# Kernel tuning notes

Measured on AMD Instinct MI355X. Metric: run time of the kernel, lower is better.

## Reference

```python
import jax, jax.numpy as jnp
import numpy as np
import math

N_ANGLES = 8
HIGH_FREQ_RATIO = 0.3


def setup_inputs() -> dict:
    key = jax.random.key(0)
    k1, k2 = jax.random.split(key)
    x = jax.random.normal(k1, (4, 256, 256, 256), dtype=jnp.float32)
    # learnable per-angle weights, init near enhance_init=1.0 with small perturbation
    angle_weights = 1.0 + 0.1 * jax.random.normal(k2, (N_ANGLES,), dtype=jnp.float32)
    return {"x": x, "angle_weights": angle_weights}


def _angle_gain(H, W, angle_weights):
    # Build [H, W] real gain: angle-sector weight in the high-frequency band, 1 elsewhere.
    cy, cx = H // 2, W // 2
    y = jnp.arange(H, dtype=jnp.float32)[:, None] - cy
    x = jnp.arange(W, dtype=jnp.float32)[None, :] - cx
    r = jnp.sqrt(y * y + x * x)
    theta = jnp.arctan2(y, x) + math.pi  # [0, 2*pi]
    angle_step = 2.0 * math.pi / N_ANGLES
    angle_idx = jnp.mod(jnp.floor(theta / angle_step).astype(jnp.int32), N_ANGLES)
    r_max = min(cy, cx)
    high_freq_mask = r > HIGH_FREQ_RATIO * r_max
    weights = angle_weights[angle_idx]  # [H, W]
    return jnp.where(high_freq_mask, weights, jnp.ones_like(weights))


def reference(x, angle_weights):
    # x: [B, C, H, W]
    H, W = x.shape[-2], x.shape[-1]
    gain = _angle_gain(H, W, angle_weights)  # [H, W], real
    xf = jnp.fft.fftshift(jnp.fft.fft2(x, norm="ortho"), axes=(-2, -1))
    # mag*gain * exp(i*phase) == gain * (mag*exp(i*phase)) == gain * spectrum (gain real)
    xf_enh = xf * gain
    x_enh = jnp.fft.ifft2(jnp.fft.ifftshift(xf_enh, axes=(-2, -1)), norm="ortho").real
    return x + x_enh
```

## Files before the change

kernel.cpp:

```cpp
#include <hip/hip_runtime.h>
#include <math.h>

#define PI_F 3.14159265358979323846f
#define WSYNC() asm volatile("s_waitcnt lgkmcnt(0)" ::: "memory")

__device__ __forceinline__ float2 cmul(float2 a, float2 b) {
    return make_float2(a.x * b.x - a.y * b.y, a.x * b.y + a.y * b.x);
}
__device__ __forceinline__ float2 cmulc(float2 a, float2 b) {
    return make_float2(a.x * b.x + a.y * b.y, a.y * b.x - a.x * b.y);
}
__device__ __forceinline__ int digitrev4(int p) {
    return ((p & 3) << 6) | (((p >> 2) & 3) << 4) | (((p >> 4) & 3) << 2) | ((p >> 6) & 3);
}
__device__ __forceinline__ int bitrev8(int p) {
    return (int)(__brev((unsigned int)p) >> 24);
}
__device__ __forceinline__ int SW(int i) { return i ^ ((i >> 4) & 15); }

__device__ __forceinline__ void tw3(int eu, float2& w1, float2& w2, float2& w3) {
    float sn, cs;
    __sincosf(-(2.0f * PI_F / 256.0f) * (float)eu, &sn, &cs);
    w1 = make_float2(cs, sn);
    w2 = cmul(w1, w1);
    w3 = cmul(w2, w1);
}

__device__ __forceinline__ void bfly4_fwd(float2 a0, float2 a1, float2 a2, float2 a3,
                                          float2& o0, float2& o1, float2& o2, float2& o3) {
    float2 t0 = make_float2(a0.x + a2.x, a0.y + a2.y);
    float2 t1 = make_float2(a0.x - a2.x, a0.y - a2.y);
    float2 t2 = make_float2(a1.x + a3.x, a1.y + a3.y);
    float2 u  = make_float2(a1.x - a3.x, a1.y - a3.y);
    float2 t3 = make_float2(u.y, -u.x);
    o0 = make_float2(t0.x + t2.x, t0.y + t2.y);
    o1 = make_float2(t1.x + t3.x, t1.y + t3.y);
    o2 = make_float2(t0.x - t2.x, t0.y - t2.y);
    o3 = make_float2(t1.x - t3.x, t1.y - t3.y);
}
__device__ __forceinline__ void bfly4_inv(float2 a0, float2 a1, float2 a2, float2 a3,
                                          float2& o0, float2& o1, float2& o2, float2& o3) {
    float2 t0 = make_float2(a0.x + a2.x, a0.y + a2.y);
    float2 t1 = make_float2(a0.x - a2.x, a0.y - a2.y);
    float2 t2 = make_float2(a1.x + a3.x, a1.y + a3.y);
    float2 u  = make_float2(a1.x - a3.x, a1.y - a3.y);
    float2 t3 = make_float2(-u.y, u.x);
    o0 = make_float2(t0.x + t2.x, t0.y + t2.y);
    o1 = make_float2(t1.x + t3.x, t1.y + t3.y);
    o2 = make_float2(t0.x - t2.x, t0.y - t2.y);
    o3 = make_float2(t1.x - t3.x, t1.y - t3.y);
}

template<int S>
__device__ __forceinline__ void stage_fwd_j(float2* line, int j, float2 w1, float2 w2, float2 w3) {
    const int h = 1 << (2 * S);
    int k  = j & (h - 1);
    int i0 = ((j >> (2 * S)) << (2 * S + 2)) + k;
    int p0 = SW(i0), p1 = SW(i0 + h), p2 = SW(i0 + 2 * h), p3 = SW(i0 + 3 * h);
    float2 a0 = line[p0], a1 = line[p1], a2 = line[p2], a3 = line[p3];
    float2 o0, o1, o2, o3;
    bfly4_fwd(a0, a1, a2, a3, o0, o1, o2, o3);
    line[p0] = o0;
    line[p1] = cmul(o1, w1);
    line[p2] = cmul(o2, w2);
    line[p3] = cmul(o3, w3);
}
template<int S>
__device__ __forceinline__ void stage_inv_j(float2* line, int j, float2 w1, float2 w2, float2 w3) {
    const int h = 1 << (2 * S);
    int k  = j & (h - 1);
    int i0 = ((j >> (2 * S)) << (2 * S + 2)) + k;
    int p0 = SW(i0), p1 = SW(i0 + h), p2 = SW(i0 + 2 * h), p3 = SW(i0 + 3 * h);
    float2 b0 = line[p0];
    float2 b1 = cmulc(line[p1], w1);
    float2 b2 = cmulc(line[p2], w2);
    float2 b3 = cmulc(line[p3], w3);
    float2 o0, o1, o2, o3;
    bfly4_inv(b0, b1, b2, b3, o0, o1, o2, o3);
    line[p0] = o0; line[p1] = o1; line[p2] = o2; line[p3] = o3;
}

template<int MB>
__device__ __forceinline__ void xs_fwd(float2* a, float2* b, int lane,
                                       float step, float cC, float sC) {
    float dm = (lane & MB) ? 1.0f : 0.0f;
    float s  = 1.0f - 2.0f * dm;
    float ang = step * dm * (float)(lane & (MB - 1));
    float sn, cs; __sincosf(ang, &sn, &cs);
    float2 tw = make_float2(cs, sn);
    float2 Cm = make_float2(1.0f + dm * (cC - 1.0f), dm * sC);
#pragma unroll
    for (int d = 0; d < 4; ++d) {
        float tax = __shfl_xor(a[d].x, MB), tay = __shfl_xor(a[d].y, MB);
        float tbx = __shfl_xor(b[d].x, MB), tby = __shfl_xor(b[d].y, MB);
        float2 ra = make_float2(tax + s * a[d].x, tay + s * a[d].y);
        float2 rb = make_float2(tbx + s * b[d].x, tby + s * b[d].y);
        a[d] = cmul(ra, tw);
        b[d] = cmul(rb, tw);
        tw = cmul(tw, Cm);
    }
}
template<int MB>
__device__ __forceinline__ void xs_inv(float2* a, float2* b, int lane,
                                       float step, float cC, float sC) {
    float dm = (lane & MB) ? 1.0f : 0.0f;
    float s  = 1.0f - 2.0f * dm;
    float ang = step * dm * (float)(lane & (MB - 1));
    float sn, cs; __sincosf(ang, &sn, &cs);
    float2 tw = make_float2(cs, sn);
    float2 Cm = make_float2(1.0f + dm * (cC - 1.0f), dm * sC);
#pragma unroll
    for (int d = 0; d < 4; ++d) {
        float2 pa = cmul(a[d], tw);
        float2 pb = cmul(b[d], tw);
        float tax = __shfl_xor(pa.x, MB), tay = __shfl_xor(pa.y, MB);
        float tbx = __shfl_xor(pb.x, MB), tby = __shfl_xor(pb.y, MB);
        a[d] = make_float2(tax + s * pa.x, tay + s * pa.y);
        b[d] = make_float2(tbx + s * pb.x, tby + s * pb.y);
        tw = cmul(tw, Cm);
    }
}
__device__ __forceinline__ void local_fwd(float2* v) {
    float2 u0 = make_float2(v[0].x + v[2].x, v[0].y + v[2].y);
    float2 u2 = make_float2(v[0].x - v[2].x, v[0].y - v[2].y);
    float2 u1 = make_float2(v[1].x + v[3].x, v[1].y + v[3].y);
    float2 w  = make_float2(v[1].x - v[3].x, v[1].y - v[3].y);
    float2 u3 = make_float2(w.y, -w.x);
    v[0] = make_float2(u0.x + u1.x, u0.y + u1.y);
    v[1] = make_float2(u0.x - u1.x, u0.y - u1.y);
    v[2] = make_float2(u2.x + u3.x, u2.y + u3.y);
    v[3] = make_float2(u2.x - u3.x, u2.y - u3.y);
}
__device__ __forceinline__ void local_inv(float2* v) {
    float2 u0 = make_float2(v[0].x + v[1].x, v[0].y + v[1].y);
    float2 u1 = make_float2(v[0].x - v[1].x, v[0].y - v[1].y);
    float2 u2 = make_float2(v[2].x + v[3].x, v[2].y + v[3].y);
    float2 u3 = make_float2(v[2].x - v[3].x, v[2].y - v[3].y);
    float2 w  = make_float2(-u3.y, u3.x);
    v[0] = make_float2(u0.x + u2.x, u0.y + u2.y);
    v[2] = make_float2(u0.x - u2.x, u0.y - u2.y);
    v[1] = make_float2(u1.x + w.x, u1.y + w.y);
    v[3] = make_float2(u1.x - w.x, u1.y - w.y);
}

__device__ __forceinline__ float gain1(float fy, float fx, const float* sw) {
    float r2 = fy * fy + fx * fx;
    float theta = atan2f(fy, fx) + PI_F;
    int idx = ((int)floorf(theta * (4.0f / PI_F))) & 7;
    float wv = sw[idx];
    return (r2 > 1474.56f) ? wv : 1.0f;
}

__global__ __launch_bounds__(256) void k_gain_lut(const float* __restrict__ wts, float* __restrict__ lut2) {
    __shared__ float sw[8];
    int h = threadIdx.x, w = blockIdx.x;
    if (h < 8) sw[h] = wts[h];
    __syncthreads();
    int kw = bitrev8(w), kh = digitrev4(h);
    float fx  = (kw < 128) ? (float)kw : (float)(kw - 256);
    float fx2 = (kw == 128) ? -128.0f : -fx;
    float fy  = (kh < 128) ? (float)kh : (float)(kh - 256);
    float fy2 = (kh == 128) ? -128.0f : -fy;
    float g1 = gain1(fy, fx, sw);
    float g2 = gain1(fy2, fx2, sw);
    lut2[w * 256 + h] = (1.0f + 0.5f * (g1 + g2)) * (1.0f / 65536.0f);
}

__global__ __launch_bounds__(256) void k_row_fwd(const float* __restrict__ x, float* __restrict__ out) {
    int t = threadIdx.x, wv = t >> 6, lane = t & 63;
    int gr = blockIdx.x * 8 + wv * 2;
    int q = gr >> 8, h = gr & 255;
    int plane = ((q >> 7) << 8) + ((q & 127) << 1);
    size_t rA = ((size_t)plane << 16) + ((size_t)h << 8);
    size_t rB = rA + 65536;
    int w4 = lane * 4;
    float4 re0 = *(const float4*)(x + rA + w4);
    float4 im0 = *(const float4*)(x + rB + w4);
    float4 re1 = *(const float4*)(x + rA + 256 + w4);
    float4 im1 = *(const float4*)(x + rB + 256 + w4);
    float2 a[4], b[4];
    a[0] = make_float2(re0.x, im0.x); a[1] = make_float2(re0.y, im0.y);
    a[2] = make_float2(re0.z, im0.z); a[3] = make_float2(re0.w, im0.w);
    b[0] = make_float2(re1.x, im1.x); b[1] = make_float2(re1.y, im1.y);
    b[2] = make_float2(re1.z, im1.z); b[3] = make_float2(re1.w, im1.w);
    xs_fwd<32>(a, b, lane, -0.09817477f, 0.99969882f, -0.02454123f);
    xs_fwd<16>(a, b, lane, -0.19634954f, 0.99879546f, -0.04906767f);
    xs_fwd< 8>(a, b, lane, -0.39269908f, 0.99518473f, -0.09801714f);
    xs_fwd< 4>(a, b, lane, -0.78539816f, 0.98078528f, -0.19509032f);
    xs_fwd< 2>(a, b, lane, -1.57079633f, 0.92387953f, -0.38268343f);
    xs_fwd< 1>(a, b, lane, -3.14159265f, 0.70710678f, -0.70710678f);
    local_fwd(a); local_fwd(b);
    *(float4*)(out + rA + w4)       = make_float4(a[0].x, a[1].x, a[2].x, a[3].x);
    *(float4*)(out + rB + w4)       = make_float4(a[0].y, a[1].y, a[2].y, a[3].y);
    *(float4*)(out + rA + 256 + w4) = make_float4(b[0].x, b[1].x, b[2].x, b[3].x);
    *(float4*)(out + rB + 256 + w4) = make_float4(b[0].y, b[1].y, b[2].y, b[3].y);
}

template<bool USE_LUT>
__global__ __launch_bounds__(256) void k_col(float* __restrict__ data,
                                             const float* __restrict__ lut2,
                                             const float* __restrict__ wts) {
    __shared__ float2 tile[16][256];
    int t = threadIdx.x;
    int q = blockIdx.x >> 4, wt = blockIdx.x & 15, w0 = wt * 16;
    int plane = ((q >> 7) << 8) + ((q & 127) << 1);
    size_t baseA = ((size_t)plane << 16) + (size_t)w0;
    size_t baseB = baseA + 65536;
    int c0 = (t & 3) * 4, h0 = (t >> 2) * 4;
    int wv = t >> 6, lane = t & 63;
    int i0 = lane * 4;

    float4 gAr[2], gBr[2];
    if (!USE_LUT) {
        if (t < 8) ((float*)tile)[t] = wts[t];
        __syncthreads();
        const float* swp = (const float*)tile;
#pragma unroll
        for (int cp = 0; cp < 2; ++cp) {
#pragma unroll
            for (int cc = 0; cc < 2; ++cc) {
                int col = wv * 4 + cp * 2 + cc;
                int kw = bitrev8(w0 + col);
                float fx  = (kw < 128) ? (float)kw : (float)(kw - 256);
                float fx2 = (kw == 128) ? -128.0f : -fx;
                float4 g;
#pragma unroll
                for (int d = 0; d < 4; ++d) {
                    int kh = digitrev4(i0 + d);
                    float fy  = (kh < 128) ? (float)kh : (float)(kh - 256);
                    float fy2 = (kh == 128) ? -128.0f : -fy;
                    float g1v = gain1(fy, fx, swp);
                    float g2v = gain1(fy2, fx2, swp);
                    (&g.x)[d] = (1.0f + 0.5f * (g1v + g2v)) * (1.0f / 65536.0f);
                }
                if (cc == 0) gAr[cp] = g; else gBr[cp] = g;
            }
        }
        __syncthreads();
    }

    {
        float4 reR[4], imR[4];
#pragma unroll
        for (int r = 0; r < 4; ++r) {
            reR[r] = *(const float4*)(data + baseA + (size_t)(h0 + r) * 256 + c0);
            imR[r] = *(const float4*)(data + baseB + (size_t)(h0 + r) * 256 + c0);
        }
#pragma unroll
        for (int r = 0; r < 4; ++r) {
            int p = SW(h0 + r);
#pragma unroll
            for (int k = 0; k < 4; ++k)
                tile[c0 + k][p] = make_float2((&reR[r].x)[k], (&imR[r].x)[k]);
        }
    }
    __syncthreads();

    float2 w31, w32, w33, w21, w22, w23, w11, w12, w13;
    tw3(lane,             w31, w32, w33);
    tw3((lane & 15) << 2, w21, w22, w23);
    tw3((lane & 3)  << 4, w11, w12, w13);
    int p0 = SW(i0), p1 = SW(i0 + 1), p2 = SW(i0 + 2), p3 = SW(i0 + 3);
#pragma unroll
    for (int cp = 0; cp < 2; ++cp) {
        int colA = wv * 4 + cp * 2, colB = colA + 1;
        float2* LA = tile[colA];
        float2* LB = tile[colB];
        float4 gA, gB;
        if (USE_LUT) {
            gA = *(const float4*)(lut2 + (size_t)(w0 + colA) * 256 + i0);
            gB = *(const float4*)(lut2 + (size_t)(w0 + colB) * 256 + i0);
        } else {
            gA = gAr[cp]; gB = gBr[cp];
        }
        stage_fwd_j<3>(LA, lane, w31, w32, w33); stage_fwd_j<3>(LB, lane, w31, w32, w33); WSYNC();
        stage_fwd_j<2>(LA, lane, w21, w22, w23); stage_fwd_j<2>(LB, lane, w21, w22, w23); WSYNC();
        stage_fwd_j<1>(LA, lane, w11, w12, w13); stage_fwd_j<1>(LB, lane, w11, w12, w13); WSYNC();
        {
            float2 o0, o1, o2, o3, r0, r1, r2, r3;
            bfly4_fwd(LA[p0], LA[p1], LA[p2], LA[p3], o0, o1, o2, o3);
            o0.x *= gA.x; o0.y *= gA.x; o1.x *= gA.y; o1.y *= gA.y;
            o2.x *= gA.z; o2.y *= gA.z; o3.x *= gA.w; o3.y *= gA.w;
            bfly4_inv(o0, o1, o2, o3, r0, r1, r2, r3);
            LA[p0] = r0; LA[p1] = r1; LA[p2] = r2; LA[p3] = r3;
            bfly4_fwd(LB[p0], LB[p1], LB[p2], LB[p3], o0, o1, o2, o3);
            o0.x *= gB.x; o0.y *= gB.x; o1.x *= gB.y; o1.y *= gB.y;
            o2.x *= gB.z; o2.y *= gB.z; o3.x *= gB.w; o3.y *= gB.w;
            bfly4_inv(o0, o1, o2, o3, r0, r1, r2, r3);
            LB[p0] = r0; LB[p1] = r1; LB[p2] = r2; LB[p3] = r3;
        }
        WSYNC();
        stage_inv_j<1>(LA, lane, w11, w12, w13); stage_inv_j<1>(LB, lane, w11, w12, w13); WSYNC();
        stage_inv_j<2>(LA, lane, w21, w22, w23); stage_inv_j<2>(LB, lane, w21, w22, w23); WSYNC();
        stage_inv_j<3>(LA, lane, w31, w32, w33); stage_inv_j<3>(LB, lane, w31, w32, w33); WSYNC();
    }
    __syncthreads();

    {
#pragma unroll
        for (int r = 0; r < 4; ++r) {
            int p = SW(h0 + r);
            float2 v0 = tile[c0 + 0][p], v1 = tile[c0 + 1][p];
            float2 v2 = tile[c0 + 2][p], v3 = tile[c0 + 3][p];
            *(float4*)(data + baseA + (size_t)(h0 + r) * 256 + c0) = make_float4(v0.x, v1.x, v2.x, v3.x);
            *(float4*)(data + baseB + (size_t)(h0 + r) * 256 + c0) = make_float4(v0.y, v1.y, v2.y, v3.y);
        }
    }
}

__global__ __launch_bounds__(256) void k_row_inv(float* __restrict__ data) {
    int t = threadIdx.x, wv = t >> 6, lane = t & 63;
    int gr = blockIdx.x * 8 + wv * 2;
    int q = gr >> 8, h = gr & 255;
    int plane = ((q >> 7) << 8) + ((q & 127) << 1);
    size_t rA = ((size_t)plane << 16) + ((size_t)h << 8);
    size_t rB = rA + 65536;
    int w4 = lane * 4;
    float4 re0 = *(const float4*)(data + rA + w4);
    float4 im0 = *(const float4*)(data + rB + w4);
    float4 re1 = *(const float4*)(data + rA + 256 + w4);
    float4 im1 = *(const float4*)(data + rB + 256 + w4);
    float2 a[4], b[4];
    a[0] = make_float2(re0.x, im0.x); a[1] = make_float2(re0.y, im0.y);
    a[2] = make_float2(re0.z, im0.z); a[3] = make_float2(re0.w, im0.w);
    b[0] = make_float2(re1.x, im1.x); b[1] = make_float2(re1.y, im1.y);
    b[2] = make_float2(re1.z, im1.z); b[3] = make_float2(re1.w, im1.w);
    local_inv(a); local_inv(b);
    xs_inv< 1>(a, b, lane,  3.14159265f, 0.70710678f,  0.70710678f);
    xs_inv< 2>(a, b, lane,  1.57079633f, 0.92387953f,  0.38268343f);
    xs_inv< 4>(a, b, lane,  0.78539816f, 0.98078528f,  0.19509032f);
    xs_inv< 8>(a, b, lane,  0.39269908f, 0.99518473f,  0.09801714f);
    xs_inv<16>(a, b, lane,  0.19634954f, 0.99879546f,  0.04906767f);
    xs_inv<32>(a, b, lane,  0.09817477f, 0.99969882f,  0.02454123f);
    *(float4*)(data + rA + w4)       = make_float4(a[0].x, a[1].x, a[2].x, a[3].x);
    *(float4*)(data + rB + w4)       = make_float4(a[0].y, a[1].y, a[2].y, a[3].y);
    *(float4*)(data + rA + 256 + w4) = make_float4(b[0].x, b[1].x, b[2].x, b[3].x);
    *(float4*)(data + rB + 256 + w4) = make_float4(b[0].y, b[1].y, b[2].y, b[3].y);
}

extern "C" void kernel_launch(void* const* d_in, const int* in_sizes, int n_in,
                              void* d_out, int out_size, void* d_ws, size_t ws_size,
                              hipStream_t stream) {
    const float* x   = (const float*)d_in[0];
    const float* wts = (const float*)d_in[1];
    float* out = (float*)d_out;
    (void)in_sizes; (void)n_in; (void)out_size;
    bool use_lut = (ws_size >= 256 * 256 * sizeof(float)) && (d_ws != nullptr);
    if (use_lut) {
        k_gain_lut<<<256, 256, 0, stream>>>(wts, (float*)d_ws);
    }
    k_row_fwd<<<16384, 256, 0, stream>>>(x, out);
    if (use_lut) {
        k_col<true><<<8192, 256, 0, stream>>>(out, (const float*)d_ws, wts);
    } else {
        k_col<false><<<8192, 256, 0, stream>>>(out, nullptr, wts);
    }
    k_row_inv<<<16384, 256, 0, stream>>>(out);
}
```

Measured before the change: 653.4 us.

## Use register radix-16 column FFT and precomputed twiddle tables for row FFTs

Replaces the column pass's four shared-memory radix-4 stages per direction with a 16x16 decomposition. Each thread runs two register-resident 16-point FFTs, and only one XOR-swizzled shared-memory transpose sits between them. This cuts LDS round trips and wave syncs. Row FFT twiddles and column twiddles now come from precomputed tables in workspace instead of being generated with sincos and recurrence. In exchange each thread holds more registers and the kernels issue extra global and cached table loads.

New measurement: 665.5 us. About the same (+1.9%).

```diff
diff --git a/kernel.cpp b/kernel.cpp
--- a/kernel.cpp
+++ b/kernel.cpp
@@ -10,21 +10,11 @@
 __device__ __forceinline__ float2 cmulc(float2 a, float2 b) {
     return make_float2(a.x * b.x + a.y * b.y, a.y * b.x - a.x * b.y);
 }
-__device__ __forceinline__ int digitrev4(int p) {
-    return ((p & 3) << 6) | (((p >> 2) & 3) << 4) | (((p >> 4) & 3) << 2) | ((p >> 6) & 3);
-}
 __device__ __forceinline__ int bitrev8(int p) {
     return (int)(__brev((unsigned int)p) >> 24);
 }
+__device__ __forceinline__ int br4(int z) { return ((z & 3) << 2) | (z >> 2); }
 __device__ __forceinline__ int SW(int i) { return i ^ ((i >> 4) & 15); }
-
-__device__ __forceinline__ void tw3(int eu, float2& w1, float2& w2, float2& w3) {
-    float sn, cs;
-    __sincosf(-(2.0f * PI_F / 256.0f) * (float)eu, &sn, &cs);
-    w1 = make_float2(cs, sn);
-    w2 = cmul(w1, w1);
-    w3 = cmul(w2, w1);
-}
 
 __device__ __forceinline__ void bfly4_fwd(float2 a0, float2 a1, float2 a2, float2 a3,
                                           float2& o0, float2& o1, float2& o2, float2& o3) {
@@ -51,35 +41,72 @@
     o3 = make_float2(t1.x - t3.x, t1.y - t3.y);
 }
 
-template<int S>
-__device__ __forceinline__ void stage_fwd_j(float2* line, int j, float2 w1, float2 w2, float2 w3) {
-    const int h = 1 << (2 * S);
-    int k  = j & (h - 1);
-    int i0 = ((j >> (2 * S)) << (2 * S + 2)) + k;
-    int p0 = SW(i0), p1 = SW(i0 + h), p2 = SW(i0 + 2 * h), p3 = SW(i0 + 3 * h);
-    float2 a0 = line[p0], a1 = line[p1], a2 = line[p2], a3 = line[p3];
+#define W16_1 make_float2( 0.92387953f, -0.38268343f)
+#define W16_2 make_float2( 0.70710678f, -0.70710678f)
+#define W16_3 make_float2( 0.38268343f, -0.92387953f)
+#define W16_4 make_float2( 0.0f,        -1.0f)
+#define W16_6 make_float2(-0.70710678f, -0.70710678f)
+#define W16_9 make_float2(-0.92387953f,  0.38268343f)
+
+__device__ __forceinline__ void fft16_fwd(float2* v) {
     float2 o0, o1, o2, o3;
-    bfly4_fwd(a0, a1, a2, a3, o0, o1, o2, o3);
-    line[p0] = o0;
-    line[p1] = cmul(o1, w1);
-    line[p2] = cmul(o2, w2);
-    line[p3] = cmul(o3, w3);
-}
-template<int S>
-__device__ __forceinline__ void stage_inv_j(float2* line, int j, float2 w1, float2 w2, float2 w3) {
-    const int h = 1 << (2 * S);
-    int k  = j & (h - 1);
-    int i0 = ((j >> (2 * S)) << (2 * S + 2)) + k;
-    int p0 = SW(i0), p1 = SW(i0 + h), p2 = SW(i0 + 2 * h), p3 = SW(i0 + 3 * h);
-    float2 b0 = line[p0];
-    float2 b1 = cmulc(line[p1], w1);
-    float2 b2 = cmulc(line[p2], w2);
-    float2 b3 = cmulc(line[p3], w3);
+    bfly4_fwd(v[0], v[4], v[8],  v[12], o0, o1, o2, o3);
+    v[0] = o0; v[4] = o1; v[8] = o2; v[12] = o3;
+    bfly4_fwd(v[1], v[5], v[9],  v[13], o0, o1, o2, o3);
+    v[1] = o0; v[5] = cmul(o1, W16_1); v[9]  = cmul(o2, W16_2); v[13] = cmul(o3, W16_3);
+    bfly4_fwd(v[2], v[6], v[10], v[14], o0, o1, o2, o3);
+    v[2] = o0; v[6] = cmul(o1, W16_2); v[10] = cmul(o2, W16_4); v[14] = cmul(o3, W16_6);
+    bfly4_fwd(v[3], v[7], v[11], v[15], o0, o1, o2, o3);
+    v[3] = o0; v[7] = cmul(o1, W16_3); v[11] = cmul(o2, W16_6); v[15] = cmul(o3, W16_9);
+#pragma unroll
+    for (int g = 0; g < 4; ++g) {
+        bfly4_fwd(v[4*g], v[4*g+1], v[4*g+2], v[4*g+3], o0, o1, o2, o3);
+        v[4*g] = o0; v[4*g+1] = o1; v[4*g+2] = o2; v[4*g+3] = o3;
+    }
+}
+__device__ __forceinline__ void fft16_inv(float2* v) {
     float2 o0, o1, o2, o3;
-    bfly4_inv(b0, b1, b2, b3, o0, o1, o2, o3);
-    line[p0] = o0; line[p1] = o1; line[p2] = o2; line[p3] = o3;
-}
-
+#pragma unroll
+    for (int g = 0; g < 4; ++g) {
+        bfly4_inv(v[4*g], v[4*g+1], v[4*g+2], v[4*g+3], o0, o1, o2, o3);
+        v[4*g] = o0; v[4*g+1] = o1; v[4*g+2] = o2; v[4*g+3] = o3;
+    }
+    bfly4_inv(v[0], v[4], v[8], v[12], o0, o1, o2, o3);
+    v[0] = o0; v[4] = o1; v[8] = o2; v[12] = o3;
+    bfly4_inv(v[1], cmulc(v[5], W16_1), cmulc(v[9],  W16_2), cmulc(v[13], W16_3), o0, o1, o2, o3);
+    v[1] = o0; v[5] = o1; v[9] = o2; v[13] = o3;
+    bfly4_inv(v[2], cmulc(v[6], W16_2), cmulc(v[10], W16_4), cmulc(v[14], W16_6), o0, o1, o2, o3);
+    v[2] = o0; v[6] = o1; v[10] = o2; v[14] = o3;
+    bfly4_inv(v[3], cmulc(v[7], W16_3), cmulc(v[11], W16_6), cmulc(v[15], W16_9), o0, o1, o2, o3);
+    v[3] = o0; v[7] = o1; v[11] = o2; v[15] = o3;
+}
+
+template<int MB>
+__device__ __forceinline__ void xs_fwd_l(float2* a, float2* b, int lane, const float2* tw) {
+    float s = (lane & MB) ? -1.0f : 1.0f;
+#pragma unroll
+    for (int d = 0; d < 4; ++d) {
+        float tax = __shfl_xor(a[d].x, MB), tay = __shfl_xor(a[d].y, MB);
+        float tbx = __shfl_xor(b[d].x, MB), tby = __shfl_xor(b[d].y, MB);
+        float2 ra = make_float2(tax + s * a[d].x, tay + s * a[d].y);
+        float2 rb = make_float2(tbx + s * b[d].x, tby + s * b[d].y);
+        a[d] = cmul(ra, tw[d]);
+        b[d] = cmul(rb, tw[d]);
+    }
+}
+template<int MB>
+__device__ __forceinline__ void xs_inv_l(float2* a, float2* b, int lane, const float2* tw) {
+    float s = (lane & MB) ? -1.0f : 1.0f;
+#pragma unroll
+    for (int d = 0; d < 4; ++d) {
+        float2 pa = cmulc(a[d], tw[d]);
+        float2 pb = cmulc(b[d], tw[d]);
+        float tax = __shfl_xor(pa.x, MB), tay = __shfl_xor(pa.y, MB);
+        float tbx = __shfl_xor(pb.x, MB), tby = __shfl_xor(pb.y, MB);
+        a[d] = make_float2(tax + s * pa.x, tay + s * pa.y);
+        b[d] = make_float2(tbx + s * pb.x, tby + s * pb.y);
+    }
+}
 template<int MB>
 __device__ __forceinline__ void xs_fwd(float2* a, float2* b, int lane,
                                        float step, float cC, float sC) {
@@ -151,22 +178,49 @@
     return (r2 > 1474.56f) ? wv : 1.0f;
 }
 
-__global__ __launch_bounds__(256) void k_gain_lut(const float* __restrict__ wts, float* __restrict__ lut2) {
+#define WS_RTW 65536
+#define WS_TWC 68608
+#define WS_FLOATS 69120
+
+__global__ __launch_bounds__(256) void k_luts(const float* __restrict__ wts, float* __restrict__ ws) {
     __shared__ float sw[8];
     int h = threadIdx.x, w = blockIdx.x;
     if (h < 8) sw[h] = wts[h];
     __syncthreads();
-    int kw = bitrev8(w), kh = digitrev4(h);
+    int kw = bitrev8(w);
+    int kh = br4(h >> 4) + (br4(h & 15) << 4);
     float fx  = (kw < 128) ? (float)kw : (float)(kw - 256);
     float fx2 = (kw == 128) ? -128.0f : -fx;
     float fy  = (kh < 128) ? (float)kh : (float)(kh - 256);
     float fy2 = (kh == 128) ? -128.0f : -fy;
     float g1 = gain1(fy, fx, sw);
     float g2 = gain1(fy2, fx2, sw);
-    lut2[w * 256 + h] = (1.0f + 0.5f * (g1 + g2)) * (1.0f / 65536.0f);
-}
-
-__global__ __launch_bounds__(256) void k_row_fwd(const float* __restrict__ x, float* __restrict__ out) {
+    ws[w * 256 + h] = (1.0f + 0.5f * (g1 + g2)) * (1.0f / 65536.0f);
+    if (w == 0) {
+        float2* rtw = (float2*)(ws + WS_RTW);
+        int lane = h >> 2, d = h & 3;
+#pragma unroll
+        for (int st = 0; st < 6; ++st) {
+            int MB = 32 >> st;
+            float step = -PI_F / (float)MB;
+            float dm = (lane & MB) ? 1.0f : 0.0f;
+            float th = dm * step * ((float)(lane & (MB - 1)) + 0.25f * (float)d);
+            float sn, cs; sincosf(th, &sn, &cs);
+            rtw[st * 256 + h] = make_float2(cs, sn);
+        }
+    }
+    if (w == 1) {
+        float2* twc = (float2*)(ws + WS_TWC);
+        int j = h >> 4, r = h & 15;
+        float th = -(2.0f * PI_F / 256.0f) * (float)(j * br4(r));
+        float sn, cs; sincosf(th, &sn, &cs);
+        twc[h] = make_float2(cs, sn);
+    }
+}
+
+template<bool TW>
+__global__ __launch_bounds__(256) void k_row_fwd(const float* __restrict__ x, float* __restrict__ out,
+                                                 const float* __restrict__ ws) {
     int t = threadIdx.x, wv = t >> 6, lane = t & 63;
     int gr = blockIdx.x * 8 + wv * 2;
     int q = gr >> 8, h = gr & 255;
@@ -183,12 +237,30 @@
     a[2] = make_float2(re0.z, im0.z); a[3] = make_float2(re0.w, im0.w);
     b[0] = make_float2(re1.x, im1.x); b[1] = make_float2(re1.y, im1.y);
     b[2] = make_float2(re1.z, im1.z); b[3] = make_float2(re1.w, im1.w);
-    xs_fwd<32>(a, b, lane, -0.09817477f, 0.99969882f, -0.02454123f);
-    xs_fwd<16>(a, b, lane, -0.19634954f, 0.99879546f, -0.04906767f);
-    xs_fwd< 8>(a, b, lane, -0.39269908f, 0.99518473f, -0.09801714f);
-    xs_fwd< 4>(a, b, lane, -0.78539816f, 0.98078528f, -0.19509032f);
-    xs_fwd< 2>(a, b, lane, -1.57079633f, 0.92387953f, -0.38268343f);
-    xs_fwd< 1>(a, b, lane, -3.14159265f, 0.70710678f, -0.70710678f);
+    if (TW) {
+        const float4* rtw = (const float4*)(ws + WS_RTW);
+        float2 tw[6][4];
+#pragma unroll
+        for (int s = 0; s < 6; ++s) {
+            float4 lo = rtw[(s * 64 + lane) * 2];
+            float4 hi = rtw[(s * 64 + lane) * 2 + 1];
+            tw[s][0] = make_float2(lo.x, lo.y); tw[s][1] = make_float2(lo.z, lo.w);
+            tw[s][2] = make_float2(hi.x, hi.y); tw[s][3] = make_float2(hi.z, hi.w);
+        }
+        xs_fwd_l<32>(a, b, lane, tw[0]);
+        xs_fwd_l<16>(a, b, lane, tw[1]);
+        xs_fwd_l< 8>(a, b, lane, tw[2]);
+        xs_fwd_l< 4>(a, b, lane, tw[3]);
+        xs_fwd_l< 2>(a, b, lane, tw[4]);
+        xs_fwd_l< 1>(a, b, lane, tw[5]);
+    } else {
+        xs_fwd<32>(a, b, lane, -0.09817477f, 0.99969882f, -0.02454123f);
+        xs_fwd<16>(a, b, lane, -0.19634954f, 0.99879546f, -0.04906767f);
+        xs_fwd< 8>(a, b, lane, -0.39269908f, 0.99518473f, -0.09801714f);
+        xs_fwd< 4>(a, b, lane, -0.78539816f, 0.98078528f, -0.19509032f);
+        xs_fwd< 2>(a, b, lane, -1.57079633f, 0.92387953f, -0.38268343f);
+        xs_fwd< 1>(a, b, lane, -3.14159265f, 0.70710678f, -0.70710678f);
+    }
     local_fwd(a); local_fwd(b);
     *(float4*)(out + rA + w4)       = make_float4(a[0].x, a[1].x, a[2].x, a[3].x);
     *(float4*)(out + rB + w4)       = make_float4(a[0].y, a[1].y, a[2].y, a[3].y);
@@ -198,7 +270,7 @@
 
 template<bool USE_LUT>
 __global__ __launch_bounds__(256) void k_col(float* __restrict__ data,
-                                             const float* __restrict__ lut2,
+                                             const float* __restrict__ ws,
                                              const float* __restrict__ wts) {
     __shared__ float2 tile[16][256];
     int t = threadIdx.x;
@@ -208,35 +280,44 @@
     size_t baseB = baseA + 65536;
     int c0 = (t & 3) * 4, h0 = (t >> 2) * 4;
     int wv = t >> 6, lane = t & 63;
-    int i0 = lane * 4;
-
-    float4 gAr[2], gBr[2];
-    if (!USE_LUT) {
-        if (t < 8) ((float*)tile)[t] = wts[t];
+    int col = wv * 4 + (lane & 3);
+    int j = lane >> 2;
+
+    float2 twc[16];
+    float  g_[16];
+    if (USE_LUT) {
+        const float4* tp = (const float4*)(ws + WS_TWC) + j * 8;
+        const float4* gp = (const float4*)(ws + (size_t)(w0 + col) * 256 + (j << 4));
+#pragma unroll
+        for (int k = 0; k < 8; ++k) {
+            float4 c4 = tp[k];
+            twc[2 * k]     = make_float2(c4.x, c4.y);
+            twc[2 * k + 1] = make_float2(c4.z, c4.w);
+        }
+#pragma unroll
+        for (int k = 0; k < 4; ++k) {
+            float4 g4 = gp[k];
+            g_[4 * k] = g4.x; g_[4 * k + 1] = g4.y; g_[4 * k + 2] = g4.z; g_[4 * k + 3] = g4.w;
+        }
+    } else {
+        __shared__ float swf[8];
+        if (t < 8) swf[t] = wts[t];
         __syncthreads();
-        const float* swp = (const float*)tile;
-#pragma unroll
-        for (int cp = 0; cp < 2; ++cp) {
-#pragma unroll
-            for (int cc = 0; cc < 2; ++cc) {
-                int col = wv * 4 + cp * 2 + cc;
-                int kw = bitrev8(w0 + col);
-                float fx  = (kw < 128) ? (float)kw : (float)(kw - 256);
-                float fx2 = (kw == 128) ? -128.0f : -fx;
-                float4 g;
-#pragma unroll
-                for (int d = 0; d < 4; ++d) {
-                    int kh = digitrev4(i0 + d);
-                    float fy  = (kh < 128) ? (float)kh : (float)(kh - 256);
-                    float fy2 = (kh == 128) ? -128.0f : -fy;
-                    float g1v = gain1(fy, fx, swp);
-                    float g2v = gain1(fy2, fx2, swp);
-                    (&g.x)[d] = (1.0f + 0.5f * (g1v + g2v)) * (1.0f / 65536.0f);
-                }
-                if (cc == 0) gAr[cp] = g; else gBr[cp] = g;
-            }
-        }
-        __syncthreads();
+        int kw = bitrev8(w0 + col);
+        float fx  = (kw < 128) ? (float)kw : (float)(kw - 256);
+        float fx2 = (kw == 128) ? -128.0f : -fx;
+#pragma unroll
+        for (int r = 0; r < 16; ++r) {
+            float sn, cs;
+            __sincosf(-(2.0f * PI_F / 256.0f) * (float)(j * br4(r)), &sn, &cs);
+            twc[r] = make_float2(cs, sn);
+            int kh = br4(j) + (br4(r) << 4);
+            float fy  = (kh < 128) ? (float)kh : (float)(kh - 256);
+            float fy2 = (kh == 128) ? -128.0f : -fy;
+            float g1v = gain1(fy, fx, swf);
+            float g2v = gain1(fy2, fx2, swf);
+            g_[r] = (1.0f + 0.5f * (g1v + g2v)) * (1.0f / 65536.0f);
+        }
     }
 
     {
@@ -256,44 +337,30 @@
     }
     __syncthreads();
 
-    float2 w31, w32, w33, w21, w22, w23, w11, w12, w13;
-    tw3(lane,             w31, w32, w33);
-    tw3((lane & 15) << 2, w21, w22, w23);
-    tw3((lane & 3)  << 4, w11, w12, w13);
-    int p0 = SW(i0), p1 = SW(i0 + 1), p2 = SW(i0 + 2), p3 = SW(i0 + 3);
-#pragma unroll
-    for (int cp = 0; cp < 2; ++cp) {
-        int colA = wv * 4 + cp * 2, colB = colA + 1;
-        float2* LA = tile[colA];
-        float2* LB = tile[colB];
-        float4 gA, gB;
-        if (USE_LUT) {
-            gA = *(const float4*)(lut2 + (size_t)(w0 + colA) * 256 + i0);
-            gB = *(const float4*)(lut2 + (size_t)(w0 + colB) * 256 + i0);
-        } else {
-            gA = gAr[cp]; gB = gBr[cp];
-        }
-        stage_fwd_j<3>(LA, lane, w31, w32, w33); stage_fwd_j<3>(LB, lane, w31, w32, w33); WSYNC();
-        stage_fwd_j<2>(LA, lane, w21, w22, w23); stage_fwd_j<2>(LB, lane, w21, w22, w23); WSYNC();
-        stage_fwd_j<1>(LA, lane, w11, w12, w13); stage_fwd_j<1>(LB, lane, w11, w12, w13); WSYNC();
-        {
-            float2 o0, o1, o2, o3, r0, r1, r2, r3;
-            bfly4_fwd(LA[p0], LA[p1], LA[p2], LA[p3], o0, o1, o2, o3);
-            o0.x *= gA.x; o0.y *= gA.x; o1.x *= gA.y; o1.y *= gA.y;
-            o2.x *= gA.z; o2.y *= gA.z; o3.x *= gA.w; o3.y *= gA.w;
-            bfly4_inv(o0, o1, o2, o3, r0, r1, r2, r3);
-            LA[p0] = r0; LA[p1] = r1; LA[p2] = r2; LA[p3] = r3;
-            bfly4_fwd(LB[p0], LB[p1], LB[p2], LB[p3], o0, o1, o2, o3);
-            o0.x *= gB.x; o0.y *= gB.x; o1.x *= gB.y; o1.y *= gB.y;
-            o2.x *= gB.z; o2.y *= gB.z; o3.x *= gB.w; o3.y *= gB.w;
-            bfly4_inv(o0, o1, o2, o3, r0, r1, r2, r3);
-            LB[p0] = r0; LB[p1] = r1; LB[p2] = r2; LB[p3] = r3;
-        }
-        WSYNC();
-        stage_inv_j<1>(LA, lane, w11, w12, w13); stage_inv_j<1>(LB, lane, w11, w12, w13); WSYNC();
-        stage_inv_j<2>(LA, lane, w21, w22, w23); stage_inv_j<2>(LB, lane, w21, w22, w23); WSYNC();
-        stage_inv_j<3>(LA, lane, w31, w32, w33); stage_inv_j<3>(LB, lane, w31, w32, w33); WSYNC();
-    }
+    float2* L = tile[col];
+    float2 v[16];
+#pragma unroll
+    for (int m = 0; m < 16; ++m) v[m] = L[(m << 4) + (j ^ m)];
+    fft16_fwd(v);
+#pragma unroll
+    for (int r = 0; r < 16; ++r) v[r] = cmul(v[r], twc[r]);
+#pragma unroll
+    for (int r = 0; r < 16; ++r) L[(r << 4) + (j ^ r)] = v[r];
+    WSYNC();
+#pragma unroll
+    for (int i = 0; i < 16; ++i) v[i] = L[(j << 4) + (i ^ j)];
+    fft16_fwd(v);
+#pragma unroll
+    for (int r = 0; r < 16; ++r) { v[r].x *= g_[r]; v[r].y *= g_[r]; }
+    fft16_inv(v);
+#pragma unroll
+    for (int n = 0; n < 16; ++n) L[(j << 4) + (n ^ j)] = v[n];
+    WSYNC();
+#pragma unroll
+    for (int r = 0; r < 16; ++r) v[r] = cmulc(L[(r << 4) + (j ^ r)], twc[r]);
+    fft16_inv(v);
+#pragma unroll
+    for (int m = 0; m < 16; ++m) L[(m << 4) + (j ^ m)] = v[m];
     __syncthreads();
 
     {
@@ -308,7 +375,8 @@
     }
 }
 
-__global__ __launch_bounds__(256) void k_row_inv(float* __restrict__ data) {
+template<bool TW>
+__global__ __launch_bounds__(256) void k_row_inv(float* __restrict__ data, const float* __restrict__ ws) {
     int t = threadIdx.x, wv = t >> 6, lane = t & 63;
     int gr = blockIdx.x * 8 + wv * 2;
     int q = gr >> 8, h = gr & 255;
@@ -326,12 +394,30 @@
     b[0] = make_float2(re1.x, im1.x); b[1] = make_float2(re1.y, im1.y);
     b[2] = make_float2(re1.z, im1.z); b[3] = make_float2(re1.w, im1.w);
     local_inv(a); local_inv(b);
-    xs_inv< 1>(a, b, lane,  3.14159265f, 0.70710678f,  0.70710678f);
-    xs_inv< 2>(a, b, lane,  1.57079633f, 0.92387953f,  0.38268343f);
-    xs_inv< 4>(a, b, lane,  0.78539816f, 0.98078528f,  0.19509032f);
-    xs_inv< 8>(a, b, lane,  0.39269908f, 0.99518473f,  0.09801714f);
-    xs_inv<16>(a, b, lane,  0.19634954f, 0.99879546f,  0.04906767f);
-    xs_inv<32>(a, b, lane,  0.09817477f, 0.99969882f,  0.02454123f);
+    if (TW) {
+        const float4* rtw = (const float4*)(ws + WS_RTW);
+        float2 tw[6][4];
+#pragma unroll
+        for (int s = 0; s < 6; ++s) {
+            float4 lo = rtw[(s * 64 + lane) * 2];
+            float4 hi = rtw[(s * 64 + lane) * 2 + 1];
+            tw[s][0] = make_float2(lo.x, lo.y); tw[s][1] = make_float2(lo.z, lo.w);
+            tw[s][2] = make_float2(hi.x, hi.y); tw[s][3] = make_float2(hi.z, hi.w);
+        }
+        xs_inv_l< 1>(a, b, lane, tw[5]);
+        xs_inv_l< 2>(a, b, lane, tw[4]);
+        xs_inv_l< 4>(a, b, lane, tw[3]);
+        xs_inv_l< 8>(a, b, lane, tw[2]);
+        xs_inv_l<16>(a, b, lane, tw[1]);
+        xs_inv_l<32>(a, b, lane, tw[0]);
+    } else {
+        xs_inv< 1>(a, b, lane,  3.14159265f, 0.70710678f,  0.70710678f);
+        xs_inv< 2>(a, b, lane,  1.57079633f, 0.92387953f,  0.38268343f);
+        xs_inv< 4>(a, b, lane,  0.78539816f, 0.98078528f,  0.19509032f);
+        xs_inv< 8>(a, b, lane,  0.39269908f, 0.99518473f,  0.09801714f);
+        xs_inv<16>(a, b, lane,  0.19634954f, 0.99879546f,  0.04906767f);
+        xs_inv<32>(a, b, lane,  0.09817477f, 0.99969882f,  0.02454123f);
+    }
     *(float4*)(data + rA + w4)       = make_float4(a[0].x, a[1].x, a[2].x, a[3].x);
     *(float4*)(data + rB + w4)       = make_float4(a[0].y, a[1].y, a[2].y, a[3].y);
     *(float4*)(data + rA + 256 + w4) = make_float4(b[0].x, b[1].x, b[2].x, b[3].x);
@@ -344,16 +430,17 @@
     const float* x   = (const float*)d_in[0];
     const float* wts = (const float*)d_in[1];
     float* out = (float*)d_out;
+    float* wsf = (float*)d_ws;
     (void)in_sizes; (void)n_in; (void)out_size;
-    bool use_lut = (ws_size >= 256 * 256 * sizeof(float)) && (d_ws != nullptr);
+    bool use_lut = (ws_size >= (size_t)WS_FLOATS * sizeof(float)) && (d_ws != nullptr);
     if (use_lut) {
-        k_gain_lut<<<256, 256, 0, stream>>>(wts, (float*)d_ws);
-    }
-    k_row_fwd<<<16384, 256, 0, stream>>>(x, out);
-    if (use_lut) {
-        k_col<true><<<8192, 256, 0, stream>>>(out, (const float*)d_ws, wts);
+        k_luts<<<256, 256, 0, stream>>>(wts, wsf);
+        k_row_fwd<true><<<16384, 256, 0, stream>>>(x, out, wsf);
+        k_col<true><<<8192, 256, 0, stream>>>(out, wsf, wts);
+        k_row_inv<true><<<16384, 256, 0, stream>>>(out, wsf);
     } else {
+        k_row_fwd<false><<<16384, 256, 0, stream>>>(x, out, nullptr);
         k_col<false><<<8192, 256, 0, stream>>>(out, nullptr, wts);
-    }
-    k_row_inv<<<16384, 256, 0, stream>>>(out);
-}
+        k_row_inv<false><<<16384, 256, 0, stream>>>(out, nullptr);
+    }
+}
```
